# Optimization experiments

Measured on AMD Instinct MI355X. Metric: run time of the kernel, lower is better.

The kernel has to match this reference:

```python
import jax, jax.numpy as jnp
import numpy as np

B, N, C = 8, 1025, 1024
H = 8
D = C // H  # 128
LORA = 16
TOK = 1024

def setup_inputs() -> dict:
    key = jax.random.key(0)
    ks = jax.random.split(key, 16)
    s = 0.02
    return {
        "x": jax.random.normal(ks[0], (B, N, C), jnp.float32),
        "style_k": jax.random.normal(ks[1], (B, N, C), jnp.float32),
        "style_v": jax.random.normal(ks[2], (B, N, C), jnp.float32),
        "W_qkv": jax.random.normal(ks[3], (C, 3 * C), jnp.float32) * s,
        "W_proj": jax.random.normal(ks[4], (C, C), jnp.float32) * s,
        "b_proj": jnp.zeros((C,), jnp.float32),
        "ak": jax.random.normal(ks[5], (TOK, LORA), jnp.float32) * s,
        "bk": jax.random.normal(ks[6], (LORA, C), jnp.float32) * s,
        "av": jax.random.normal(ks[7], (TOK, LORA), jnp.float32) * s,
        "bv": jax.random.normal(ks[8], (LORA, C), jnp.float32) * s,
        "W1": jax.random.normal(ks[9], (C, C // 4), jnp.float32) * s,
        "b1": jnp.zeros((C // 4,), jnp.float32),
        "W2": jax.random.normal(ks[10], (C // 4, 1), jnp.float32) * s,
        "b2": jnp.zeros((1,), jnp.float32),
    }

def reference(x, style_k, style_v, W_qkv, W_proj, b_proj, ak, bk, av, bv, W1, b1, W2, b2):
    Bx, Nx, Cx = x.shape
    # cls-token gating MLP over transposed patch tokens: cp has shape [B, C, N-1], N-1 == C
    cls_token = x[:, :1, :]                         # [B,1,C]
    cp = jnp.transpose(x[:, 1:, :], (0, 2, 1))      # [B,C,N-1]
    h = jax.nn.relu(cp @ W1 + b1)                   # [B,C,C//4]
    attn_w = jax.nn.sigmoid(h @ W2 + b2)            # [B,C,1]
    attn_w = attn_w[..., 0][:, None, :]             # [B,1,C]
    weighted_cls = cls_token * attn_w               # [B,1,C]

    qkv = (x @ W_qkv).reshape(Bx, Nx, 3, H, D)
    q, k, v = qkv[:, :, 0], qkv[:, :, 1], qkv[:, :, 2]  # each [B,N,H,D]

    tokens_k = ak @ bk                              # [TOK, C] (TOK == C)
    tokens_v = av @ bv
    lora_k = (style_k @ tokens_k.T).reshape(Bx, Nx, H, D)
    lora_v = (style_v @ tokens_v.T).reshape(Bx, Nx, H, D)

    kk = k + lora_k
    vv = v + lora_v
    scale = D ** -0.5  # xformers default softmax scale
    scores = jnp.einsum('bqhd,bkhd->bhqk', q, kk) * scale
    attn = jax.nn.softmax(scores, axis=-1)
    out = jnp.einsum('bhqk,bkhd->bqhd', attn, vv).reshape(Bx, Nx, Cx)
    out = out @ W_proj + b_proj

    x_return = jnp.concatenate([out[:, :1, :] + weighted_cls, out[:, 1:, :]], axis=1)
    return (x_return, vv)
```

## Files before the change

kernel.cpp:

```cpp
#include <hip/hip_runtime.h>
#include <hip/hip_bf16.h>
#include <stdint.h>

#define B_ 8
#define N_ 1025
#define C_ 1024
#define H_ 8
#define D_ 128
#define TOK_ 1024
#define LORA_ 16
#define M_ 8200
#define NPAD_ 1032

using bf16x8 = __attribute__((ext_vector_type(8))) short;
using f32x4  = __attribute__((ext_vector_type(4))) float;
typedef unsigned short u16;

__device__ __forceinline__ u16 f2bf(float f) {
    union { float f; unsigned u; } v; v.f = f;
    unsigned r = v.u + 0x7fffu + ((v.u >> 16) & 1u);
    return (u16)(r >> 16);
}

__device__ __forceinline__ unsigned cvt_pk_bf16(float lo, float hi) {
    unsigned r;
    asm("v_cvt_pk_bf16_f32 %0, %1, %2" : "=v"(r) : "v"(lo), "v"(hi));
    return r;
}

__device__ __forceinline__ void gload16(const u16* g, u16* l) {
    __builtin_amdgcn_global_load_lds(
        (const __attribute__((address_space(1))) void*)g,
        (__attribute__((address_space(3))) void*)l, 16, 0, 0);
}

__device__ __forceinline__ int xcd_swz(int bid, int nwg) {
    int cpx = nwg >> 3;
    return (bid & 7) * cpx + (bid >> 3);
}
__device__ __forceinline__ int xcd_swz_g(int bid, int nwg) {
    int q = nwg >> 3, r = nwg & 7;
    int xcd = bid & 7, i = bid >> 3;
    return (xcd < r ? xcd * (q + 1) : r * (q + 1) + (xcd - r) * q) + i;
}

__global__ __launch_bounds__(256) void cast3_kernel(
    const float* __restrict__ x, const float* __restrict__ sk, const float* __restrict__ sv,
    u16* __restrict__ xb, u16* __restrict__ skb, u16* __restrict__ svb)
{
    const float* in = blockIdx.y == 0 ? x : (blockIdx.y == 1 ? sk : sv);
    u16* out = blockIdx.y == 0 ? xb : (blockIdx.y == 1 ? skb : svb);
    size_t i = (size_t)blockIdx.x * 256 + threadIdx.x;
    float4 a = *((const float4*)in + i * 2);
    float4 b = *((const float4*)in + i * 2 + 1);
    bf16x8 v;
    v[0] = (short)f2bf(a.x); v[1] = (short)f2bf(a.y);
    v[2] = (short)f2bf(a.z); v[3] = (short)f2bf(a.w);
    v[4] = (short)f2bf(b.x); v[5] = (short)f2bf(b.y);
    v[6] = (short)f2bf(b.z); v[7] = (short)f2bf(b.w);
    *(bf16x8*)(out + i * 8) = v;
}

__global__ __launch_bounds__(256) void padcast16_kernel(
    const float* __restrict__ ak, const float* __restrict__ av,
    u16* __restrict__ akp, u16* __restrict__ avp)
{
    const float* in = blockIdx.y ? av : ak;
    u16* out = blockIdx.y ? avp : akp;
    int i = blockIdx.x * 256 + threadIdx.x;
    int t = i >> 4, l = i & 15;
    out[(size_t)t * 32 + l] = f2bf(in[i]);
    out[(size_t)t * 32 + 16 + l] = 0;
}

__global__ __launch_bounds__(256) void castb_kernel(
    const float* __restrict__ bk, const float* __restrict__ bv,
    u16* __restrict__ bkb, u16* __restrict__ bvb)
{
    const float* in = blockIdx.y ? bv : bk;
    u16* out = blockIdx.y ? bvb : bkb;
    int i = blockIdx.x * 256 + threadIdx.x;
    out[i] = f2bf(in[i]);
}

__global__ __launch_bounds__(256) void lora16_mfma(
    const u16* __restrict__ skb, const u16* __restrict__ svb,
    const u16* __restrict__ bkb, const u16* __restrict__ bvb,
    u16* __restrict__ sk16p, u16* __restrict__ sv16p)
{
    const u16* sb = blockIdx.y ? svb : skb;
    const u16* bb = blockIdx.y ? bvb : bkb;
    u16* op = blockIdx.y ? sv16p : sk16p;
    const int lane = threadIdx.x & 63, wid = threadIdx.x >> 6;
    const int base = blockIdx.x * 64 + wid * 16;
    int ma = base + (lane & 15); if (ma > M_ - 1) ma = M_ - 1;
    const int l = lane & 15;
    const u16* arow = sb + (size_t)ma * C_ + (lane >> 4) * 8;
    const u16* brow = bb + (size_t)l * C_ + (lane >> 4) * 8;
    f32x4 acc = {0.f, 0.f, 0.f, 0.f};
#pragma unroll
    for (int k0 = 0; k0 < C_; k0 += 32) {
        bf16x8 af = *(const bf16x8*)(arow + k0);
        bf16x8 bf = *(const bf16x8*)(brow + k0);
        acc = __builtin_amdgcn_mfma_f32_16x16x32_bf16(af, bf, acc, 0, 0, 0);
    }
#pragma unroll
    for (int r = 0; r < 4; ++r) {
        int m = base + (lane >> 4) * 4 + r; if (m > M_ - 1) m = M_ - 1;
        op[(size_t)m * 32 + l] = f2bf(acc[r]);
        op[(size_t)m * 32 + 16 + l] = 0;
    }
}

__global__ __launch_bounds__(256) void wt_kernel(
    const float* __restrict__ in, u16* __restrict__ out, int K, int Nw)
{
    __shared__ float t[32][33];
    int n0 = blockIdx.x * 32, k0 = blockIdx.y * 32;
    int tx = threadIdx.x & 31, ty = threadIdx.x >> 5;
#pragma unroll
    for (int yy = 0; yy < 32; yy += 8)
        t[ty + yy][tx] = in[(size_t)(k0 + ty + yy) * Nw + n0 + tx];
    __syncthreads();
#pragma unroll
    for (int yy = 0; yy < 32; yy += 8)
        out[(size_t)(n0 + ty + yy) * K + k0 + tx] = f2bf(t[tx][ty + yy]);
}

__global__ __launch_bounds__(256) void xt_kernel(
    const float* __restrict__ x, u16* __restrict__ xT)
{
    __shared__ float tb[32][33];
    int t0 = blockIdx.x * 32, c0 = blockIdx.y * 32, b = blockIdx.z;
    int tx = threadIdx.x & 31, ty = threadIdx.x >> 5;
#pragma unroll
    for (int yy = 0; yy < 32; yy += 8)
        tb[ty + yy][tx] = x[((size_t)b * N_ + 1 + t0 + ty + yy) * C_ + c0 + tx];
    __syncthreads();
#pragma unroll
    for (int yy = 0; yy < 32; yy += 8)
        xT[((size_t)b * 1024 + c0 + ty + yy) * 1024 + t0 + tx] = f2bf(tb[tx][ty + yy]);
}

__global__ __launch_bounds__(256) void vvt_kernel(
    const float* __restrict__ vv, u16* __restrict__ vvT)
{
    __shared__ float t[32][33];
    int n0 = blockIdx.x * 32, d0 = blockIdx.y * 32, bh = blockIdx.z;
    int b = bh >> 3, h = bh & 7;
    int tx = threadIdx.x & 31, ty = threadIdx.x >> 5;
#pragma unroll
    for (int yy = 0; yy < 32; yy += 8) {
        int n = n0 + ty + yy; if (n > 1024) n = 1024;
        t[ty + yy][tx] = vv[((size_t)(b * N_) + n) * C_ + h * D_ + d0 + tx];
    }
    __syncthreads();
#pragma unroll
    for (int yy = 0; yy < 32; yy += 8) {
        int n = n0 + tx;
        if (n < NPAD_)
            vvT[((size_t)bh * D_ + d0 + ty + yy) * NPAD_ + n] = f2bf(t[tx][ty + yy]);
    }
}

__device__ __forceinline__ void stage_tile(
    const u16* __restrict__ base, int row0, int maxrow,
    u16* lds, int k0, int lane, int wid)
{
#pragma unroll
    for (int j = 0; j < 4; ++j) {
        int i = wid * 4 + j;
        int p = i * 1024 + 16 * lane;
        int row = p >> 7, cb = p & 127;
        int cbs = cb ^ ((row & 7) << 4);
        int gr = row0 + row; if (gr > maxrow) gr = maxrow;
        gload16(base + (size_t)gr * 1024 + k0 + (cbs >> 1), lds + i * 512);
    }
}

__device__ __forceinline__ void gemm_pass(
    const u16* __restrict__ A, const u16* __restrict__ Bt, int row0, int nb0,
    u16* As, u16* Bs, f32x4 acc[4][4],
    const int lane, const int wid, const int wr, const int wc)
{
    for (int k0 = 0; k0 < 1024; k0 += 64) {
        __syncthreads();
        stage_tile(A,  row0, M_ - 1,    As, k0, lane, wid);
        stage_tile(Bt, nb0,  (1 << 30), Bs, k0, lane, wid);
        __syncthreads();
#pragma unroll
        for (int ks = 0; ks < 2; ++ks) {
            bf16x8 af[4], bfr[4];
#pragma unroll
            for (int mi = 0; mi < 4; ++mi) {
                int r = wr * 64 + mi * 16 + (lane & 15);
                int byte = (r * 128 + ks * 64 + (lane >> 4) * 16) ^ ((r & 7) << 4);
                af[mi] = *(const bf16x8*)((const char*)As + byte);
            }
#pragma unroll
            for (int ni = 0; ni < 4; ++ni) {
                int r = wc * 64 + ni * 16 + (lane & 15);
                int byte = (r * 128 + ks * 64 + (lane >> 4) * 16) ^ ((r & 7) << 4);
                bfr[ni] = *(const bf16x8*)((const char*)Bs + byte);
            }
#pragma unroll
            for (int mi = 0; mi < 4; ++mi)
#pragma unroll
                for (int ni = 0; ni < 4; ++ni)
                    acc[mi][ni] = __builtin_amdgcn_mfma_f32_16x16x32_bf16(
                        af[mi], bfr[ni], acc[mi][ni], 0, 0, 0);
        }
    }
}

template<int NSEG>
__device__ __forceinline__ void stage_tile512(
    const u16* __restrict__ base, int row0, int maxrow,
    u16* lds, int k0, int lane, int wid)
{
#pragma unroll
    for (int j = 0; j < NSEG; ++j) {
        int i = wid * NSEG + j;
        int p = i * 1024 + 16 * lane;
        int row = p >> 7, cb = p & 127;
        int cbs = cb ^ ((row & 7) << 4);
        int gr = row0 + row; if (gr > maxrow) gr = maxrow;
        gload16(base + (size_t)gr * 1024 + k0 + (cbs >> 1), lds + i * 512);
    }
}

__device__ __forceinline__ void gemm_pass512(
    const u16* __restrict__ A, const u16* __restrict__ Bt, int row0, int nb0,
    u16* As, u16* Bs, f32x4 acc[4][4],
    const int lane, const int wid, const int wr, const int wc)
{
    for (int k0 = 0; k0 < 1024; k0 += 64) {
        __syncthreads();
        stage_tile512<2>(A,  row0, M_ - 1,    As, k0, lane, wid);
        stage_tile512<4>(Bt, nb0,  (1 << 30), Bs, k0, lane, wid);
        __syncthreads();
#pragma unroll
        for (int ks = 0; ks < 2; ++ks) {
            bf16x8 af[4], bfr[4];
#pragma unroll
            for (int mi = 0; mi < 4; ++mi) {
                int r = wr * 64 + mi * 16 + (lane & 15);
                int byte = (r * 128 + ks * 64 + (lane >> 4) * 16) ^ ((r & 7) << 4);
                af[mi] = *(const bf16x8*)((const char*)As + byte);
            }
#pragma unroll
            for (int ni = 0; ni < 4; ++ni) {
                int r = wc * 64 + ni * 16 + (lane & 15);
                int byte = (r * 128 + ks * 64 + (lane >> 4) * 16) ^ ((r & 7) << 4);
                bfr[ni] = *(const bf16x8*)((const char*)Bs + byte);
            }
#pragma unroll
            for (int mi = 0; mi < 4; ++mi)
#pragma unroll
                for (int ni = 0; ni < 4; ++ni)
                    acc[mi][ni] = __builtin_amdgcn_mfma_f32_16x16x32_bf16(
                        af[mi], bfr[ni], acc[mi][ni], 0, 0, 0);
        }
    }
}

__global__ __launch_bounds__(256) void se_gemm(
    const u16* __restrict__ xT, const u16* __restrict__ W1T,
    const float* __restrict__ b1, const float* __restrict__ W2,
    float* __restrict__ gred)
{
    __shared__ u16 As[8192], Bs[8192];
    __shared__ float red[128];
    const int tid = threadIdx.x, lane = tid & 63, wid = tid >> 6;
    const int wr = wid >> 1, wc = wid & 1;
    const int row0 = blockIdx.x * 128;
    const int pass = blockIdx.y;
    if (tid < 128) red[tid] = 0.f;
    const f32x4 FZ = {0.f, 0.f, 0.f, 0.f};

    f32x4 acc[4][4];
#pragma unroll
    for (int mi = 0; mi < 4; ++mi)
#pragma unroll
        for (int ni = 0; ni < 4; ++ni) acc[mi][ni] = FZ;
    gemm_pass(xT, W1T, row0, pass * 128, As, Bs, acc, lane, wid, wr, wc);
#pragma unroll
    for (int mi = 0; mi < 4; ++mi) {
#pragma unroll
        for (int r = 0; r < 4; ++r) {
            float v = 0.f;
#pragma unroll
            for (int ni = 0; ni < 4; ++ni) {
                int j = pass * 128 + wc * 64 + ni * 16 + (lane & 15);
                float h = acc[mi][ni][r] + b1[j];
                v += fmaxf(h, 0.f) * W2[j];
            }
#pragma unroll
            for (int off = 1; off < 16; off <<= 1) v += __shfl_xor(v, off);
            if ((lane & 15) == 0)
                atomicAdd(&red[wr * 64 + mi * 16 + (lane >> 4) * 4 + r], v);
        }
    }
    __syncthreads();
    if (tid < 128) atomicAdd(&gred[row0 + tid], red[tid]);
}

__global__ __launch_bounds__(256) void se_fin(
    const float* __restrict__ gred, const float* __restrict__ b2,
    const float* __restrict__ x, float* __restrict__ wcls)
{
    int row = blockIdx.x * 256 + threadIdx.x;
    int b = row >> 10, c = row & 1023;
    wcls[row] = x[(size_t)b * N_ * C_ + c] / (1.f + expf(-(gred[row] + b2[0])));
}

__global__ __launch_bounds__(512) void qkv_gemm(
    const u16* __restrict__ xb, const u16* __restrict__ WqkvT,
    const u16* __restrict__ sk16p, const u16* __restrict__ sv16p,
    const u16* __restrict__ akp, const u16* __restrict__ avp,
    u16* __restrict__ qb, u16* __restrict__ kkb, float* __restrict__ vvout)
{
    __shared__ u16 As[8192], Bs[16384];
    const int tid = threadIdx.x, lane = tid & 63, wid = tid >> 6;
    const int wr = wid >> 2, wc = wid & 3;
    const int swz = xcd_swz_g(blockIdx.x, 65 * 12);
    const int row0 = (swz / 12) * 128;
    const int ct = swz % 12, region = ct >> 2;
    const int creg = (ct & 3) * 256;
    const f32x4 FZ = {0.f, 0.f, 0.f, 0.f};
    f32x4 acc[4][4];
#pragma unroll
    for (int mi = 0; mi < 4; ++mi)
#pragma unroll
        for (int ni = 0; ni < 4; ++ni) acc[mi][ni] = FZ;

    gemm_pass512(xb, WqkvT, row0, region * 1024 + creg, As, Bs, acc, lane, wid, wr, wc);

    if (region >= 1) {
        const u16* a16 = (region == 1) ? sk16p : sv16p;
        const u16* b16 = (region == 1) ? akp : avp;
        bf16x8 af2[4], bf2v[4];
#pragma unroll
        for (int mi = 0; mi < 4; ++mi) {
            int gr = row0 + wr * 64 + mi * 16 + (lane & 15);
            if (gr > M_ - 1) gr = M_ - 1;
            af2[mi] = *(const bf16x8*)(a16 + (size_t)gr * 32 + (lane >> 4) * 8);
        }
#pragma unroll
        for (int ni = 0; ni < 4; ++ni) {
            int gc = creg + wc * 64 + ni * 16 + (lane & 15);
            bf2v[ni] = *(const bf16x8*)(b16 + (size_t)gc * 32 + (lane >> 4) * 8);
        }
#pragma unroll
        for (int mi = 0; mi < 4; ++mi)
#pragma unroll
            for (int ni = 0; ni < 4; ++ni)
                acc[mi][ni] = __builtin_amdgcn_mfma_f32_16x16x32_bf16(
                    af2[mi], bf2v[ni], acc[mi][ni], 0, 0, 0);
    }

    const float QSCALE = 0.1275006182f;
#pragma unroll
    for (int mi = 0; mi < 4; ++mi) {
#pragma unroll
        for (int r = 0; r < 4; ++r) {
            int gr = row0 + wr * 64 + mi * 16 + (lane >> 4) * 4 + r;
            if (gr >= M_) continue;
#pragma unroll
            for (int ni = 0; ni < 4; ++ni) {
                int gc = creg + wc * 64 + ni * 16 + (lane & 15);
                float v = acc[mi][ni][r];
                if (region == 0)      qb [(size_t)gr * C_ + gc] = f2bf(v * QSCALE);
                else if (region == 1) kkb[(size_t)gr * C_ + gc] = f2bf(v);
                else                  vvout[(size_t)gr * C_ + gc] = v;
            }
        }
    }
}

__global__ __launch_bounds__(512) void proj_gemm(
    const u16* __restrict__ ob, const u16* __restrict__ WprojT,
    const float* __restrict__ bias, const float* __restrict__ wcls,
    float* __restrict__ outp)
{
    __shared__ u16 As[8192], Bs[16384];
    const int tid = threadIdx.x, lane = tid & 63, wid = tid >> 6;
    const int wr = wid >> 2, wc = wid & 3;
    const int swz = xcd_swz_g(blockIdx.x, 65 * 4);
    const int row0 = (swz / 4) * 128;
    const int ct = swz % 4;
    const f32x4 FZ = {0.f, 0.f, 0.f, 0.f};
    f32x4 acc[4][4];
#pragma unroll
    for (int mi = 0; mi < 4; ++mi)
#pragma unroll
        for (int ni = 0; ni < 4; ++ni) acc[mi][ni] = FZ;

    gemm_pass512(ob, WprojT, row0, ct * 256, As, Bs, acc, lane, wid, wr, wc);

#pragma unroll
    for (int mi = 0; mi < 4; ++mi) {
#pragma unroll
        for (int r = 0; r < 4; ++r) {
            int gr = row0 + wr * 64 + mi * 16 + (lane >> 4) * 4 + r;
            if (gr >= M_) continue;
#pragma unroll
            for (int ni = 0; ni < 4; ++ni) {
                int gc = ct * 256 + wc * 64 + ni * 16 + (lane & 15);
                float v = acc[mi][ni][r] + bias[gc];
                if (gr % N_ == 0) v += wcls[(gr / N_) * C_ + gc];
                outp[(size_t)gr * C_ + gc] = v;
            }
        }
    }
}

__device__ __forceinline__ int psw(int pr, int colb) {
    return (pr * 128 + colb) ^ ((pr & 7) << 4) ^ ((pr & 8) << 2);
}

__global__ __launch_bounds__(256) void attn_kernel(
    const u16* __restrict__ qb, const u16* __restrict__ kkb,
    const u16* __restrict__ vvT, u16* __restrict__ ob)
{
    __shared__ u16 Ks[8192];
    __shared__ u16 Vs[8192];
    __shared__ u16 Ps[4096];
    const int tid = threadIdx.x, lane = tid & 63, wid = tid >> 6;
    const int swz = xcd_swz(blockIdx.x, 17 * 64);
    const int qt = swz % 17, bh = swz / 17, b = bh >> 3, h = bh & 7;
    const int n0q = qt * 64;
    const float THR = 11.54f;
    const u16* kbase = kkb + (size_t)b * N_ * C_ + h * D_;
    const u16* vbase = vvT + (size_t)bh * D_ * NPAD_;

    bf16x8 qf[4];
    {
        int qrow = n0q + wid * 16 + (lane & 15); if (qrow > 1024) qrow = 1024;
        const u16* qbase = qb + (size_t)(b * N_ + qrow) * C_ + h * D_ + (lane >> 4) * 8;
#pragma unroll
        for (int ks = 0; ks < 4; ++ks) qf[ks] = *(const bf16x8*)(qbase + ks * 32);
    }

    const int rowK = wid * 16 + (lane >> 4);
    const int cbsE = ((lane & 15) * 16) ^ ((rowK & 7) << 4);
    const u16* kpe = kbase + (size_t)rowK * C_ + (cbsE >> 1);
    const u16* kpo = kbase + (size_t)(rowK + 4) * C_ + ((cbsE ^ 64) >> 1);
    const int rowV = wid * 32 + (lane >> 3);
    const int cbsV = ((lane & 7) * 16) ^ ((rowV & 7) << 4);
    const u16* vp = vbase + (size_t)rowV * NPAD_ + (cbsV >> 1);

    const bf16x8 ones = {0x3F80, 0x3F80, 0x3F80, 0x3F80, 0x3F80, 0x3F80, 0x3F80, 0x3F80};
    float mrow[4];
    const f32x4 FZ = {0.f, 0.f, 0.f, 0.f};
    f32x4 of[8], lsacc = FZ;
#pragma unroll
    for (int r = 0; r < 4; ++r) mrow[r] = -3e38f;
#pragma unroll
    for (int ct = 0; ct < 8; ++ct) of[ct] = FZ;

    char* psb = (char*)Ps + wid * 2048;

    for (int t = 0; t < 17; ++t) {
        __syncthreads();
        gload16(kpe,              Ks + (wid * 4 + 0) * 512);
        gload16(kpo,              Ks + (wid * 4 + 1) * 512);
        gload16(kpe + 8 * C_,     Ks + (wid * 4 + 2) * 512);
        gload16(kpo + 8 * C_,     Ks + (wid * 4 + 3) * 512);
        gload16(vp,               Vs + (wid * 4 + 0) * 512);
        gload16(vp + 8 * NPAD_,   Vs + (wid * 4 + 1) * 512);
        gload16(vp + 16 * NPAD_,  Vs + (wid * 4 + 2) * 512);
        gload16(vp + 24 * NPAD_,  Vs + (wid * 4 + 3) * 512);
        kpe += 64 * C_; kpo += 64 * C_; vp += 64;
        __syncthreads();

        f32x4 s[4];
        __builtin_amdgcn_s_setprio(1);
#pragma unroll
        for (int jt = 0; jt < 4; ++jt) {
            f32x4 a = FZ;
#pragma unroll
            for (int ks = 0; ks < 4; ++ks) {
                int kvr = jt * 16 + (lane & 15);
                int byte = (kvr * 256 + ks * 64 + (lane >> 4) * 16) ^ ((kvr & 7) << 4);
                bf16x8 kf = *(const bf16x8*)((const char*)Ks + byte);
                a = __builtin_amdgcn_mfma_f32_16x16x32_bf16(qf[ks], kf, a, 0, 0, 0);
            }
            s[jt] = a;
        }
        __builtin_amdgcn_s_setprio(0);
        if (t == 16) {
#pragma unroll
            for (int jt = 0; jt < 4; ++jt) {
                int kvglob = 1024 + jt * 16 + (lane & 15);
                if (kvglob > 1024) {
                    s[jt][0] = -3e38f; s[jt][1] = -3e38f;
                    s[jt][2] = -3e38f; s[jt][3] = -3e38f;
                }
            }
        }

        float rmax[4];
#pragma unroll
        for (int r = 0; r < 4; ++r)
            rmax[r] = fmaxf(fmaxf(s[0][r], s[1][r]), fmaxf(s[2][r], s[3][r]));
        float g = fmaxf(fmaxf(rmax[0], rmax[1]), fmaxf(rmax[2], rmax[3]));
#pragma unroll
        for (int off = 1; off < 16; off <<= 1) g = fmaxf(g, __shfl_xor(g, off));
        int need = 0;
#pragma unroll
        for (int r = 0; r < 4; ++r) need |= (g > mrow[r] + THR) ? 1 : 0;

        if (__any(need)) {
            float al[4];
#pragma unroll
            for (int r = 0; r < 4; ++r) {
                float t0 = rmax[r];
#pragma unroll
                for (int off = 1; off < 16; off <<= 1) t0 = fmaxf(t0, __shfl_xor(t0, off));
                float mn = fmaxf(mrow[r], t0);
                al[r] = exp2f(mrow[r] - mn);
                mrow[r] = mn;
            }
#pragma unroll
            for (int ct = 0; ct < 8; ++ct)
#pragma unroll
                for (int r = 0; r < 4; ++r) of[ct][r] *= al[r];
#pragma unroll
            for (int r = 0; r < 4; ++r) lsacc[r] *= al[r];
        }
#pragma unroll
        for (int jt = 0; jt < 4; ++jt)
#pragma unroll
            for (int r = 0; r < 4; ++r) s[jt][r] = exp2f(s[jt][r] - mrow[r]);

#pragma unroll
        for (int jt = 0; jt < 4; ++jt) {
            unsigned pk01 = cvt_pk_bf16(s[jt][0], s[jt][1]);
            unsigned pk23 = cvt_pk_bf16(s[jt][2], s[jt][3]);
            int colb = (jt * 16 + (lane & 15)) * 2;
            int pr0 = (lane >> 4) * 4;
            *(u16*)(psb + psw(pr0,     colb)) = (u16)pk01;
            *(u16*)(psb + psw(pr0 + 1, colb)) = (u16)(pk01 >> 16);
            *(u16*)(psb + psw(pr0 + 2, colb)) = (u16)pk23;
            *(u16*)(psb + psw(pr0 + 3, colb)) = (u16)(pk23 >> 16);
        }

        bf16x8 pa[2];
#pragma unroll
        for (int ks2 = 0; ks2 < 2; ++ks2) {
            int prr = lane & 15;
            pa[ks2] = *(const bf16x8*)(psb + psw(prr, ks2 * 64 + (lane >> 4) * 16));
        }

        __builtin_amdgcn_s_setprio(1);
        lsacc = __builtin_amdgcn_mfma_f32_16x16x32_bf16(pa[0], ones, lsacc, 0, 0, 0);
        lsacc = __builtin_amdgcn_mfma_f32_16x16x32_bf16(pa[1], ones, lsacc, 0, 0, 0);
#pragma unroll
        for (int ct = 0; ct < 8; ++ct)
#pragma unroll
            for (int ks2 = 0; ks2 < 2; ++ks2) {
                int d = ct * 16 + (lane & 15);
                int byte = (d * 128 + ks2 * 64 + (lane >> 4) * 16) ^ ((d & 7) << 4);
                bf16x8 vf = *(const bf16x8*)((const char*)Vs + byte);
                of[ct] = __builtin_amdgcn_mfma_f32_16x16x32_bf16(pa[ks2], vf, of[ct], 0, 0, 0);
            }
        __builtin_amdgcn_s_setprio(0);
    }

#pragma unroll
    for (int ct = 0; ct < 8; ++ct)
#pragma unroll
        for (int r = 0; r < 4; ++r) {
            int n = n0q + wid * 16 + (lane >> 4) * 4 + r;
            if (n <= 1024)
                ob[(size_t)(b * N_ + n) * C_ + h * D_ + ct * 16 + (lane & 15)] =
                    f2bf(of[ct][r] / lsacc[r]);
        }
}

extern "C" void kernel_launch(void* const* d_in, const int* in_sizes, int n_in,
                              void* d_out, int out_size, void* d_ws, size_t ws_size,
                              hipStream_t stream)
{
    const float* x       = (const float*)d_in[0];
    const float* style_k = (const float*)d_in[1];
    const float* style_v = (const float*)d_in[2];
    const float* W_qkv   = (const float*)d_in[3];
    const float* W_proj  = (const float*)d_in[4];
    const float* b_proj  = (const float*)d_in[5];
    const float* ak      = (const float*)d_in[6];
    const float* bk      = (const float*)d_in[7];
    const float* av      = (const float*)d_in[8];
    const float* bv      = (const float*)d_in[9];
    const float* W1      = (const float*)d_in[10];
    const float* b1      = (const float*)d_in[11];
    const float* W2      = (const float*)d_in[12];
    const float* b2      = (const float*)d_in[13];

    float* outp   = (float*)d_out;
    float* vv_out = outp + (size_t)M_ * C_;

    u16* WqkvT = (u16*)outp;
    u16* xbb   = WqkvT + (size_t)3072 * 1024;
    u16* W1T   = xbb + (size_t)M_ * C_;
    u16* akp   = W1T + (size_t)256 * 1024;
    u16* avp   = akp + 1024 * 32;
    u16* bkb   = avp + 1024 * 32;
    u16* bvb   = bkb + 16 * 1024;
    u16* sk16p = bvb + 16 * 1024;
    u16* sv16p = sk16p + (size_t)M_ * 32;

    u16* ws     = (u16*)d_ws;
    u16* qb     = ws;
    u16* kkb    = qb  + (size_t)M_ * C_;
    u16* obuf   = kkb + (size_t)M_ * C_;
    u16* vvT    = obuf + (size_t)M_ * C_;
    u16* WprojT = vvT + (size_t)B_ * H_ * D_ * NPAD_;
    float* wcls = (float*)(WprojT + (size_t)1024 * 1024);
    float* gred = wcls + 8192;
    u16* skb = obuf;
    u16* svb = vvT;
    u16* xT  = qb;

    wt_kernel<<<dim3(96, 32), 256, 0, stream>>>(W_qkv, WqkvT, 1024, 3072);
    wt_kernel<<<dim3(32, 32), 256, 0, stream>>>(W_proj, WprojT, 1024, 1024);
    wt_kernel<<<dim3(8, 32), 256, 0, stream>>>(W1, W1T, 1024, 256);
    padcast16_kernel<<<dim3(64, 2), 256, 0, stream>>>(ak, av, akp, avp);
    castb_kernel<<<dim3(64, 2), 256, 0, stream>>>(bk, bv, bkb, bvb);
    cast3_kernel<<<dim3(4100, 3), 256, 0, stream>>>(x, style_k, style_v, xbb, skb, svb);
    xt_kernel<<<dim3(32, 32, 8), 256, 0, stream>>>(x, xT);
    hipMemsetAsync(gred, 0, 8192 * sizeof(float), stream);
    se_gemm<<<dim3(64, 2), 256, 0, stream>>>(xT, W1T, b1, W2, gred);
    se_fin<<<dim3(32), 256, 0, stream>>>(gred, b2, x, wcls);
    lora16_mfma<<<dim3(129, 2), 256, 0, stream>>>(skb, svb, bkb, bvb, sk16p, sv16p);

    qkv_gemm<<<dim3(65 * 12), 512, 0, stream>>>(xbb, WqkvT, sk16p, sv16p, akp, avp,
                                                qb, kkb, vv_out);
    vvt_kernel<<<dim3(33, 4, 64), 256, 0, stream>>>(vv_out, vvT);
    attn_kernel<<<dim3(17 * 64), 256, 0, stream>>>(qb, kkb, vvT, obuf);
    proj_gemm<<<dim3(65 * 4), 512, 0, stream>>>(obuf, WprojT, b_proj, wcls, outp);
}
```

Baseline: 308.7 us.

## Rework attention kernel to 32x32x16 MFMA with register-resident P and 128-row Q tiles

```diff
diff --git a/kernel.cpp b/kernel.cpp
--- a/kernel.cpp
+++ b/kernel.cpp
@@ -14,6 +14,8 @@
 
 using bf16x8 = __attribute__((ext_vector_type(8))) short;
 using f32x4  = __attribute__((ext_vector_type(4))) float;
+using f32x16 = __attribute__((ext_vector_type(16))) float;
+using u32x4  = __attribute__((ext_vector_type(4))) unsigned;
 typedef unsigned short u16;
 
 __device__ __forceinline__ u16 f2bf(float f) {
@@ -415,167 +417,160 @@
     }
 }
 
-__device__ __forceinline__ int psw(int pr, int colb) {
-    return (pr * 128 + colb) ^ ((pr & 7) << 4) ^ ((pr & 8) << 2);
-}
-
 __global__ __launch_bounds__(256) void attn_kernel(
     const u16* __restrict__ qb, const u16* __restrict__ kkb,
     const u16* __restrict__ vvT, u16* __restrict__ ob)
 {
     __shared__ u16 Ks[8192];
     __shared__ u16 Vs[8192];
-    __shared__ u16 Ps[4096];
     const int tid = threadIdx.x, lane = tid & 63, wid = tid >> 6;
-    const int swz = xcd_swz(blockIdx.x, 17 * 64);
-    const int qt = swz % 17, bh = swz / 17, b = bh >> 3, h = bh & 7;
-    const int n0q = qt * 64;
+    const int swz = xcd_swz(blockIdx.x, 9 * 64);
+    const int qt = swz % 9, bh = swz / 9, b = bh >> 3, h = bh & 7;
+    const int n0q = qt * 128 + wid * 32;
+    const int l31 = lane & 31, hi = lane >> 5;
     const float THR = 11.54f;
     const u16* kbase = kkb + (size_t)b * N_ * C_ + h * D_;
     const u16* vbase = vvT + (size_t)bh * D_ * NPAD_;
 
-    bf16x8 qf[4];
+    bf16x8 qfB[8];
     {
-        int qrow = n0q + wid * 16 + (lane & 15); if (qrow > 1024) qrow = 1024;
-        const u16* qbase = qb + (size_t)(b * N_ + qrow) * C_ + h * D_ + (lane >> 4) * 8;
-#pragma unroll
-        for (int ks = 0; ks < 4; ++ks) qf[ks] = *(const bf16x8*)(qbase + ks * 32);
+        int qrow = n0q + l31; if (qrow > 1024) qrow = 1024;
+        const u16* qp = qb + (size_t)(b * N_ + qrow) * C_ + h * D_ + hi * 8;
+#pragma unroll
+        for (int s = 0; s < 8; ++s) qfB[s] = *(const bf16x8*)(qp + s * 16);
     }
 
     const int rowK = wid * 16 + (lane >> 4);
-    const int cbsE = ((lane & 15) * 16) ^ ((rowK & 7) << 4);
-    const u16* kpe = kbase + (size_t)rowK * C_ + (cbsE >> 1);
-    const u16* kpo = kbase + (size_t)(rowK + 4) * C_ + ((cbsE ^ 64) >> 1);
+    const int swzK = ((lane & 15) * 16) ^ ((lane >> 4) << 4);
+    const u16* kp0 = kbase + (size_t)rowK * C_ + (swzK >> 1);
+    const u16* kp1 = kbase + (size_t)(rowK + 4) * C_ + ((swzK ^ 64) >> 1);
+    const u16* kp2 = kbase + (size_t)(rowK + 8) * C_ + ((swzK ^ 32) >> 1);
+    const u16* kp3 = kbase + (size_t)(rowK + 12) * C_ + ((swzK ^ 96) >> 1);
     const int rowV = wid * 32 + (lane >> 3);
-    const int cbsV = ((lane & 7) * 16) ^ ((rowV & 7) << 4);
-    const u16* vp = vbase + (size_t)rowV * NPAD_ + (cbsV >> 1);
+    const int swzV = ((lane & 7) * 16) ^ ((lane >> 3) << 4);
+    const u16* vp0 = vbase + (size_t)rowV * NPAD_ + (swzV >> 1);
+    const u16* vp1 = vbase + (size_t)(rowV + 8) * NPAD_ + ((swzV ^ 32) >> 1);
 
     const bf16x8 ones = {0x3F80, 0x3F80, 0x3F80, 0x3F80, 0x3F80, 0x3F80, 0x3F80, 0x3F80};
-    float mrow[4];
-    const f32x4 FZ = {0.f, 0.f, 0.f, 0.f};
-    f32x4 of[8], lsacc = FZ;
-#pragma unroll
-    for (int r = 0; r < 4; ++r) mrow[r] = -3e38f;
-#pragma unroll
-    for (int ct = 0; ct < 8; ++ct) of[ct] = FZ;
-
-    char* psb = (char*)Ps + wid * 2048;
+    f32x16 of[4], lsacc;
+#pragma unroll
+    for (int i = 0; i < 16; ++i) { lsacc[i] = 0.f; of[0][i] = 0.f; of[1][i] = 0.f; of[2][i] = 0.f; of[3][i] = 0.f; }
+    float mrow = -3e38f;
+
+    u16* KsW = Ks + (size_t)wid * 4 * 512;
+    u16* VsW = Vs + (size_t)wid * 4 * 512;
 
     for (int t = 0; t < 17; ++t) {
         __syncthreads();
-        gload16(kpe,              Ks + (wid * 4 + 0) * 512);
-        gload16(kpo,              Ks + (wid * 4 + 1) * 512);
-        gload16(kpe + 8 * C_,     Ks + (wid * 4 + 2) * 512);
-        gload16(kpo + 8 * C_,     Ks + (wid * 4 + 3) * 512);
-        gload16(vp,               Vs + (wid * 4 + 0) * 512);
-        gload16(vp + 8 * NPAD_,   Vs + (wid * 4 + 1) * 512);
-        gload16(vp + 16 * NPAD_,  Vs + (wid * 4 + 2) * 512);
-        gload16(vp + 24 * NPAD_,  Vs + (wid * 4 + 3) * 512);
-        kpe += 64 * C_; kpo += 64 * C_; vp += 64;
+        gload16(kp0, KsW);        gload16(kp1, KsW + 512);
+        gload16(kp2, KsW + 1024); gload16(kp3, KsW + 1536);
+        gload16(vp0, VsW);                gload16(vp1, VsW + 512);
+        gload16(vp0 + 16 * NPAD_, VsW + 1024); gload16(vp1 + 16 * NPAD_, VsW + 1536);
+        kp0 += 64 * C_; kp1 += 64 * C_; kp2 += 64 * C_; kp3 += 64 * C_;
+        vp0 += 64; vp1 += 64;
         __syncthreads();
 
-        f32x4 s[4];
+        f32x16 s0, s1;
+#pragma unroll
+        for (int i = 0; i < 16; ++i) { s0[i] = 0.f; s1[i] = 0.f; }
+        const int kswz = ((l31 & 7) << 4) ^ ((l31 & 8) << 2);
         __builtin_amdgcn_s_setprio(1);
 #pragma unroll
-        for (int jt = 0; jt < 4; ++jt) {
-            f32x4 a = FZ;
-#pragma unroll
-            for (int ks = 0; ks < 4; ++ks) {
-                int kvr = jt * 16 + (lane & 15);
-                int byte = (kvr * 256 + ks * 64 + (lane >> 4) * 16) ^ ((kvr & 7) << 4);
-                bf16x8 kf = *(const bf16x8*)((const char*)Ks + byte);
-                a = __builtin_amdgcn_mfma_f32_16x16x32_bf16(qf[ks], kf, a, 0, 0, 0);
-            }
-            s[jt] = a;
+        for (int sl = 0; sl < 8; ++sl) {
+            int ka = (l31 * 256 + sl * 32 + hi * 16) ^ kswz;
+            bf16x8 kf0 = *(const bf16x8*)((const char*)Ks + ka);
+            bf16x8 kf1 = *(const bf16x8*)((const char*)Ks + ka + 8192);
+            s0 = __builtin_amdgcn_mfma_f32_32x32x16_bf16(kf0, qfB[sl], s0, 0, 0, 0);
+            s1 = __builtin_amdgcn_mfma_f32_32x32x16_bf16(kf1, qfB[sl], s1, 0, 0, 0);
         }
         __builtin_amdgcn_s_setprio(0);
+
         if (t == 16) {
-#pragma unroll
-            for (int jt = 0; jt < 4; ++jt) {
-                int kvglob = 1024 + jt * 16 + (lane & 15);
-                if (kvglob > 1024) {
-                    s[jt][0] = -3e38f; s[jt][1] = -3e38f;
-                    s[jt][2] = -3e38f; s[jt][3] = -3e38f;
-                }
-            }
-        }
-
-        float rmax[4];
-#pragma unroll
-        for (int r = 0; r < 4; ++r)
-            rmax[r] = fmaxf(fmaxf(s[0][r], s[1][r]), fmaxf(s[2][r], s[3][r]));
-        float g = fmaxf(fmaxf(rmax[0], rmax[1]), fmaxf(rmax[2], rmax[3]));
-#pragma unroll
-        for (int off = 1; off < 16; off <<= 1) g = fmaxf(g, __shfl_xor(g, off));
-        int need = 0;
-#pragma unroll
-        for (int r = 0; r < 4; ++r) need |= (g > mrow[r] + THR) ? 1 : 0;
-
-        if (__any(need)) {
-            float al[4];
-#pragma unroll
-            for (int r = 0; r < 4; ++r) {
-                float t0 = rmax[r];
-#pragma unroll
-                for (int off = 1; off < 16; off <<= 1) t0 = fmaxf(t0, __shfl_xor(t0, off));
-                float mn = fmaxf(mrow[r], t0);
-                al[r] = exp2f(mrow[r] - mn);
-                mrow[r] = mn;
-            }
-#pragma unroll
-            for (int ct = 0; ct < 8; ++ct)
-#pragma unroll
-                for (int r = 0; r < 4; ++r) of[ct][r] *= al[r];
-#pragma unroll
-            for (int r = 0; r < 4; ++r) lsacc[r] *= al[r];
-        }
-#pragma unroll
-        for (int jt = 0; jt < 4; ++jt)
-#pragma unroll
-            for (int r = 0; r < 4; ++r) s[jt][r] = exp2f(s[jt][r] - mrow[r]);
-
-#pragma unroll
-        for (int jt = 0; jt < 4; ++jt) {
-            unsigned pk01 = cvt_pk_bf16(s[jt][0], s[jt][1]);
-            unsigned pk23 = cvt_pk_bf16(s[jt][2], s[jt][3]);
-            int colb = (jt * 16 + (lane & 15)) * 2;
-            int pr0 = (lane >> 4) * 4;
-            *(u16*)(psb + psw(pr0,     colb)) = (u16)pk01;
-            *(u16*)(psb + psw(pr0 + 1, colb)) = (u16)(pk01 >> 16);
-            *(u16*)(psb + psw(pr0 + 2, colb)) = (u16)pk23;
-            *(u16*)(psb + psw(pr0 + 3, colb)) = (u16)(pk23 >> 16);
-        }
-
-        bf16x8 pa[2];
-#pragma unroll
-        for (int ks2 = 0; ks2 < 2; ++ks2) {
-            int prr = lane & 15;
-            pa[ks2] = *(const bf16x8*)(psb + psw(prr, ks2 * 64 + (lane >> 4) * 16));
+            const float NEG = -3e38f;
+            s0[0] = hi ? NEG : s0[0];
+#pragma unroll
+            for (int r = 1; r < 16; ++r) s0[r] = NEG;
+#pragma unroll
+            for (int r = 0; r < 16; ++r) s1[r] = NEG;
+        }
+
+        float mt = fmaxf(s0[0], s1[0]);
+#pragma unroll
+        for (int r = 1; r < 16; ++r) mt = fmaxf(mt, fmaxf(s0[r], s1[r]));
+        mt = fmaxf(mt, __shfl_xor(mt, 32));
+
+        if (__any(mt > mrow + THR)) {
+            float mn = fmaxf(mrow, mt);
+            float al = exp2f(mrow - mn);
+            mrow = mn;
+            float alr[16];
+#pragma unroll
+            for (int r = 0; r < 16; ++r)
+                alr[r] = __shfl(al, (r & 3) + 8 * (r >> 2) + 4 * hi);
+#pragma unroll
+            for (int r = 0; r < 16; ++r) {
+                of[0][r] *= alr[r]; of[1][r] *= alr[r];
+                of[2][r] *= alr[r]; of[3][r] *= alr[r];
+                lsacc[r] *= alr[r];
+            }
+        }
+#pragma unroll
+        for (int r = 0; r < 16; ++r) { s0[r] = exp2f(s0[r] - mrow); s1[r] = exp2f(s1[r] - mrow); }
+
+        bf16x8 pa[4];
+        {
+            unsigned pk[8][2], xp[8][2];
+#pragma unroll
+            for (int g = 0; g < 4; ++g) {
+                pk[g][0] = cvt_pk_bf16(s0[4 * g], s0[4 * g + 1]);
+                pk[g][1] = cvt_pk_bf16(s0[4 * g + 2], s0[4 * g + 3]);
+                pk[g + 4][0] = cvt_pk_bf16(s1[4 * g], s1[4 * g + 1]);
+                pk[g + 4][1] = cvt_pk_bf16(s1[4 * g + 2], s1[4 * g + 3]);
+            }
+#pragma unroll
+            for (int g = 0; g < 8; ++g) {
+                xp[g][0] = __shfl_xor((int)pk[g][0], 32);
+                xp[g][1] = __shfl_xor((int)pk[g][1], 32);
+            }
+#pragma unroll
+            for (int sub = 0; sub < 2; ++sub) {
+                int g0 = sub * 4;
+                u32x4 f0 = { hi ? xp[g0 + 1][0] : pk[g0][0],     hi ? xp[g0 + 1][1] : pk[g0][1],
+                             hi ? pk[g0 + 1][0] : xp[g0][0],     hi ? pk[g0 + 1][1] : xp[g0][1] };
+                u32x4 f1 = { hi ? xp[g0 + 3][0] : pk[g0 + 2][0], hi ? xp[g0 + 3][1] : pk[g0 + 2][1],
+                             hi ? pk[g0 + 3][0] : xp[g0 + 2][0], hi ? pk[g0 + 3][1] : xp[g0 + 2][1] };
+                pa[sub * 2 + 0] = __builtin_bit_cast(bf16x8, f0);
+                pa[sub * 2 + 1] = __builtin_bit_cast(bf16x8, f1);
+            }
         }
 
         __builtin_amdgcn_s_setprio(1);
-        lsacc = __builtin_amdgcn_mfma_f32_16x16x32_bf16(pa[0], ones, lsacc, 0, 0, 0);
-        lsacc = __builtin_amdgcn_mfma_f32_16x16x32_bf16(pa[1], ones, lsacc, 0, 0, 0);
-#pragma unroll
-        for (int ct = 0; ct < 8; ++ct)
-#pragma unroll
-            for (int ks2 = 0; ks2 < 2; ++ks2) {
-                int d = ct * 16 + (lane & 15);
-                int byte = (d * 128 + ks2 * 64 + (lane >> 4) * 16) ^ ((d & 7) << 4);
-                bf16x8 vf = *(const bf16x8*)((const char*)Vs + byte);
-                of[ct] = __builtin_amdgcn_mfma_f32_16x16x32_bf16(pa[ks2], vf, of[ct], 0, 0, 0);
-            }
+#pragma unroll
+        for (int ksl = 0; ksl < 4; ++ksl)
+            lsacc = __builtin_amdgcn_mfma_f32_32x32x16_bf16(pa[ksl], ones, lsacc, 0, 0, 0);
+#pragma unroll
+        for (int ksl = 0; ksl < 4; ++ksl) {
+#pragma unroll
+            for (int dsub = 0; dsub < 4; ++dsub) {
+                int va = ((dsub * 32 + l31) * 128 + ksl * 32 + hi * 16) ^ kswz;
+                bf16x8 vf = *(const bf16x8*)((const char*)Vs + va);
+                of[dsub] = __builtin_amdgcn_mfma_f32_32x32x16_bf16(pa[ksl], vf, of[dsub], 0, 0, 0);
+            }
+        }
         __builtin_amdgcn_s_setprio(0);
     }
 
-#pragma unroll
-    for (int ct = 0; ct < 8; ++ct)
-#pragma unroll
-        for (int r = 0; r < 4; ++r) {
-            int n = n0q + wid * 16 + (lane >> 4) * 4 + r;
+    float invl[16];
+#pragma unroll
+    for (int r = 0; r < 16; ++r) invl[r] = 1.f / lsacc[r];
+#pragma unroll
+    for (int dsub = 0; dsub < 4; ++dsub)
+#pragma unroll
+        for (int r = 0; r < 16; ++r) {
+            int n = n0q + (r & 3) + 8 * (r >> 2) + 4 * hi;
             if (n <= 1024)
-                ob[(size_t)(b * N_ + n) * C_ + h * D_ + ct * 16 + (lane & 15)] =
-                    f2bf(of[ct][r] / lsacc[r]);
+                ob[(size_t)(b * N_ + n) * C_ + h * D_ + dsub * 32 + l31] =
+                    f2bf(of[dsub][r] * invl[r]);
         }
 }
 
@@ -638,6 +633,6 @@
     qkv_gemm<<<dim3(65 * 12), 512, 0, stream>>>(xbb, WqkvT, sk16p, sv16p, akp, avp,
                                                 qb, kkb, vv_out);
     vvt_kernel<<<dim3(33, 4, 64), 256, 0, stream>>>(vv_out, vvT);
-    attn_kernel<<<dim3(17 * 64), 256, 0, stream>>>(qb, kkb, vvT, obuf);
+    attn_kernel<<<dim3(9 * 64), 256, 0, stream>>>(qb, kkb, vvT, obuf);
     proj_gemm<<<dim3(65 * 4), 512, 0, stream>>>(obuf, WprojT, b_proj, wcls, outp);
 }
```

Result: slower. 321.5 us (+4.2%).
